# Performance work log

Hardware: AMD Instinct MI355X
Metric: run time of the kernel (lower is better)

Reference implementation:

```python
import jax, jax.numpy as jnp
import numpy as np

N_NODES = 50000
N_EDGES = 200000
IN_FEATS = 32
OUT_FEATS = 32
EDGE_DIM = 16


def setup_inputs() -> dict:
    key = jax.random.key(0)
    k1, k2, k3, k4, k5 = jax.random.split(key, 5)
    feat = jax.random.normal(k1, (N_NODES, IN_FEATS), dtype=jnp.float32)
    efeat = jax.random.normal(k2, (N_EDGES, EDGE_DIM), dtype=jnp.float32)
    src = jax.random.randint(k3, (N_EDGES,), 0, N_NODES, dtype=jnp.int32)
    dst = jax.random.randint(k4, (N_EDGES,), 0, N_NODES, dtype=jnp.int32)
    # edge_func = Linear(EDGE_DIM -> IN_FEATS*OUT_FEATS)
    W_edge = jax.random.normal(k5, (EDGE_DIM, IN_FEATS * OUT_FEATS), dtype=jnp.float32) * (1.0 / np.sqrt(EDGE_DIM))
    b_edge = jnp.zeros((IN_FEATS * OUT_FEATS,), dtype=jnp.float32)
    bias = jnp.zeros((OUT_FEATS,), dtype=jnp.float32)
    return {"feat": feat, "efeat": efeat, "src": src, "dst": dst,
            "W_edge": W_edge, "b_edge": b_edge, "bias": bias}


def reference(feat, efeat, src, dst, W_edge, b_edge, bias):
    # edge_func: (E, edge_dim) -> (E, in, out) edge-conditioned weights
    w = (efeat @ W_edge + b_edge).reshape(-1, IN_FEATS, OUT_FEATS)
    # u_mul_e + sum over in dim  ==  per-edge matvec: h_src[e] @ W[e]
    h_src = feat[src]                               # (E, in) gather
    msg = jnp.einsum('ei,eio->eo', h_src, w)        # (E, out)
    # mean reduce over incoming edges per destination node
    agg = jax.ops.segment_sum(msg, dst, num_segments=N_NODES)   # (N, out)
    deg = jax.ops.segment_sum(jnp.ones((msg.shape[0],), dtype=msg.dtype), dst,
                              num_segments=N_NODES)
    agg = agg / jnp.maximum(deg, 1.0)[:, None]      # zero-degree nodes stay 0
    return agg + bias
```

## Files before the change

kernel.cpp:

```cpp
#include <hip/hip_runtime.h>
#include <hip/hip_bf16.h>

#define NNODES 50000
#define NEDGES 200000
#define WCT_ROW 552
#define WCT_BYTES (32 * WCT_ROW * 2)
#define HROW 40
#define TILE_EDGES 64
#define NTILES (NEDGES / TILE_EDGES)
#define GEMM_BLOCKS ((NTILES + 1) / 2)
#define CHAIN_BLKS ((NEDGES + 255) / 256)
#define DROW 33

#define MSG_OFF   0
#define HEAD_OFF  25600000
#define NEXT_OFF  25800000
#define WCT_OFF   26600000

using f32x4 = __attribute__((ext_vector_type(4))) float;
using f16x2 = __attribute__((ext_vector_type(2))) _Float16;
using f16x4 = __attribute__((ext_vector_type(4))) _Float16;
using f16x8 = __attribute__((ext_vector_type(8))) _Float16;

__device__ __forceinline__ f16x2 pkrtz(float a, float b) {
    return __builtin_bit_cast(f16x2, __builtin_amdgcn_cvt_pkrtz(a, b));
}

__device__ __forceinline__ void gload_lds16(const void* g, void* l) {
    __builtin_amdgcn_global_load_lds(
        (const __attribute__((address_space(1))) unsigned int*)g,
        (__attribute__((address_space(3))) unsigned int*)l, 16, 0, 0);
}

#define WCT_BLKS 69
__global__ void init_kernel(const float* __restrict__ W_edge,
                            const float* __restrict__ b_edge,
                            _Float16* __restrict__ wct,
                            unsigned* __restrict__ head) {
    int b = blockIdx.x;
    if (b < WCT_BLKS) {
        int gid = b * 256 + threadIdx.x;
        if (gid >= 32 * WCT_ROW) return;
        int n = gid / WCT_ROW;
        int c = gid - n * WCT_ROW;
        float v = 0.0f;
        if (c < 512)      v = W_edge[(c & 15) * 1024 + (c >> 4) * 32 + n];
        else if (c < 544) v = b_edge[(c - 512) * 32 + n];
        wct[gid] = (_Float16)v;
    } else {
        int gid = (b - WCT_BLKS) * 256 + threadIdx.x;
        if (gid < NNODES) head[gid] = 0xFFFFFFFFu;
    }
}

__global__ __launch_bounds__(256, 3) void work_kernel(
    const float* __restrict__ feat, const float* __restrict__ efeat,
    const int* __restrict__ src, const int* __restrict__ dst,
    const _Float16* __restrict__ wct_g,
    float4* __restrict__ msg4, unsigned* __restrict__ head,
    unsigned* __restrict__ next) {

    __shared__ __align__(16) unsigned short wct_lds[32 * WCT_ROW];
    __shared__ __align__(16) unsigned short h_lds[TILE_EDGES * HROW];
    __shared__ __align__(16) float dtile[TILE_EDGES * DROW];

    const int t = threadIdx.x;

    if (blockIdx.x >= GEMM_BLOCKS) {
        int e = (blockIdx.x - GEMM_BLOCKS) * 256 + t;
        if (e < NEDGES)
            next[e] = atomicExch(&head[dst[e]], (unsigned)e);
        return;
    }

    const int lane = t & 63;
    const int wave = t >> 6;
    const int tile0 = blockIdx.x * 2;
    const int tile1 = tile0 + 1;
    const bool has1 = (tile1 < NTILES);
    const int ebase0 = tile0 * TILE_EDGES;
    const int ebase1 = tile1 * TILE_EDGES;

    const int r16 = lane & 15;
    const int g   = lane >> 4;
    const int wbase = wave * 16;
    const int et = t >> 2, p = t & 3;

    {
        const char* gsrc = (const char*)wct_g;
        char* lbase = (char*)wct_lds;
        #pragma unroll
        for (int c = 0; c < 9; ++c) {
            int chunk = wave + c * 4;
            if (chunk < 35) {
                int boff = (chunk << 10) + lane * 16;
                if (boff < WCT_BYTES) gload_lds16(gsrc + boff, lbase + boff);
            }
        }
    }

    const int se0 = src[ebase0 + et];
    int se1 = 0;
    if (has1) se1 = src[ebase1 + et];

    float4 ef0a, ef0b, ef1a, ef1b;
    {
        const float* efp = efeat + (ebase0 + wbase + r16) * 16 + (g & 1) * 8;
        ef0a = *(const float4*)efp;
        ef0b = *(const float4*)(efp + 4);
    }
    if (has1) {
        const float* efp = efeat + (ebase1 + wbase + r16) * 16 + (g & 1) * 8;
        ef1a = *(const float4*)efp;
        ef1b = *(const float4*)(efp + 4);
    }

    {
        const float* fp = feat + se0 * 32 + p * 8;
        float4 a = *(const float4*)fp;
        float4 b = *(const float4*)(fp + 4);
        uint4 hp;
        hp.x = __builtin_bit_cast(unsigned int, pkrtz(a.x, a.y));
        hp.y = __builtin_bit_cast(unsigned int, pkrtz(a.z, a.w));
        hp.z = __builtin_bit_cast(unsigned int, pkrtz(b.x, b.y));
        hp.w = __builtin_bit_cast(unsigned int, pkrtz(b.z, b.w));
        *(uint4*)(void*)(h_lds + et * HROW + p * 8) = hp;
    }

    f16x2 ef2[4] = { pkrtz(ef0a.x, ef0a.y), pkrtz(ef0a.z, ef0a.w),
                     pkrtz(ef0b.x, ef0b.y), pkrtz(ef0b.z, ef0b.w) };

    __syncthreads();

    const _Float16* brow0 = (const _Float16*)wct_lds + r16 * WCT_ROW;
    const _Float16* brow1 = (const _Float16*)wct_lds + (16 + r16) * WCT_ROW;

    unsigned int hbc[16];
    f16x8 af_bias;
    {
        const uint4* hrow = (const uint4*)(void*)(h_lds + (wbase + r16) * HROW);
        unsigned int hw[16];
        #pragma unroll
        for (int q = 0; q < 4; ++q) {
            uint4 v = hrow[q];
            hw[q*4+0] = v.x; hw[q*4+1] = v.y; hw[q*4+2] = v.z; hw[q*4+3] = v.w;
        }
        const bool hi = (g >> 1) & 1;
        #pragma unroll
        for (int s = 0; s < 16; ++s) {
            unsigned int x = hi ? (hw[s] >> 16) : (hw[s] & 0xffffu);
            hbc[s] = x | (x << 16);
        }
        af_bias = *(const f16x8*)(void*)((const _Float16*)h_lds + (wbase + r16) * HROW + g * 8);
    }

    float4 f1a = {0,0,0,0}, f1b = {0,0,0,0};
    if (has1) {
        const float* fp = feat + se1 * 32 + p * 8;
        f1a = *(const float4*)fp;
        f1b = *(const float4*)(fp + 4);
    }

    f32x4 acc0 = {0.f, 0.f, 0.f, 0.f};
    f32x4 acc1 = {0.f, 0.f, 0.f, 0.f};

    #pragma unroll
    for (int s = 0; s < 16; ++s) {
        const int koff = s * 32 + g * 8;
        f16x8 b0 = *(const f16x8*)(brow0 + koff);
        f16x8 b1 = *(const f16x8*)(brow1 + koff);
        f16x2 hb = __builtin_bit_cast(f16x2, hbc[s]);
        f16x2 p0 = hb * ef2[0], p1 = hb * ef2[1], p2 = hb * ef2[2], p3 = hb * ef2[3];
        f16x4 lo  = __builtin_shufflevector(p0, p1, 0, 1, 2, 3);
        f16x4 hi4 = __builtin_shufflevector(p2, p3, 0, 1, 2, 3);
        f16x8 af  = __builtin_shufflevector(lo, hi4, 0, 1, 2, 3, 4, 5, 6, 7);
        acc0 = __builtin_amdgcn_mfma_f32_16x16x32_f16(af, b0, acc0, 0, 0, 0);
        acc1 = __builtin_amdgcn_mfma_f32_16x16x32_f16(af, b1, acc1, 0, 0, 0);
    }
    {
        const int koff = 512 + g * 8;
        f16x8 b0 = *(const f16x8*)(brow0 + koff);
        f16x8 b1 = *(const f16x8*)(brow1 + koff);
        acc0 = __builtin_amdgcn_mfma_f32_16x16x32_f16(af_bias, b0, acc0, 0, 0, 0);
        acc1 = __builtin_amdgcn_mfma_f32_16x16x32_f16(af_bias, b1, acc1, 0, 0, 0);
    }

    {
        const int browD = wbase + g * 4;
        #pragma unroll
        for (int r = 0; r < 4; ++r) {
            dtile[(browD + r) * DROW + r16]      = acc0[r];
            dtile[(browD + r) * DROW + 16 + r16] = acc1[r];
        }
    }
    asm volatile("s_waitcnt lgkmcnt(0)" ::: "memory");
    __builtin_amdgcn_sched_barrier(0);
    {
        const int rA = wbase + (lane >> 3);
        const int cA = (lane & 7) * 4;
        float4 vA = *(const float4*)(dtile + rA * DROW + cA);
        float4 vB = *(const float4*)(dtile + (rA + 8) * DROW + cA);
        float4* mp = msg4 + (size_t)ebase0 * 8 + wave * 128;
        mp[lane]      = vA;
        mp[64 + lane] = vB;
    }

    if (!has1) return;

    {
        uint4 hp;
        hp.x = __builtin_bit_cast(unsigned int, pkrtz(f1a.x, f1a.y));
        hp.y = __builtin_bit_cast(unsigned int, pkrtz(f1a.z, f1a.w));
        hp.z = __builtin_bit_cast(unsigned int, pkrtz(f1b.x, f1b.y));
        hp.w = __builtin_bit_cast(unsigned int, pkrtz(f1b.z, f1b.w));
        *(uint4*)(void*)(h_lds + et * HROW + p * 8) = hp;
    }
    asm volatile("s_waitcnt lgkmcnt(0)" ::: "memory");
    __builtin_amdgcn_sched_barrier(0);

    ef2[0] = pkrtz(ef1a.x, ef1a.y); ef2[1] = pkrtz(ef1a.z, ef1a.w);
    ef2[2] = pkrtz(ef1b.x, ef1b.y); ef2[3] = pkrtz(ef1b.z, ef1b.w);

    {
        const uint4* hrow = (const uint4*)(void*)(h_lds + (wbase + r16) * HROW);
        unsigned int hw[16];
        #pragma unroll
        for (int q = 0; q < 4; ++q) {
            uint4 v = hrow[q];
            hw[q*4+0] = v.x; hw[q*4+1] = v.y; hw[q*4+2] = v.z; hw[q*4+3] = v.w;
        }
        const bool hi = (g >> 1) & 1;
        #pragma unroll
        for (int s = 0; s < 16; ++s) {
            unsigned int x = hi ? (hw[s] >> 16) : (hw[s] & 0xffffu);
            hbc[s] = x | (x << 16);
        }
        af_bias = *(const f16x8*)(void*)((const _Float16*)h_lds + (wbase + r16) * HROW + g * 8);
    }

    acc0 = (f32x4){0.f, 0.f, 0.f, 0.f};
    acc1 = (f32x4){0.f, 0.f, 0.f, 0.f};

    #pragma unroll
    for (int s = 0; s < 16; ++s) {
        const int koff = s * 32 + g * 8;
        f16x8 b0 = *(const f16x8*)(brow0 + koff);
        f16x8 b1 = *(const f16x8*)(brow1 + koff);
        f16x2 hb = __builtin_bit_cast(f16x2, hbc[s]);
        f16x2 p0 = hb * ef2[0], p1 = hb * ef2[1], p2 = hb * ef2[2], p3 = hb * ef2[3];
        f16x4 lo  = __builtin_shufflevector(p0, p1, 0, 1, 2, 3);
        f16x4 hi4 = __builtin_shufflevector(p2, p3, 0, 1, 2, 3);
        f16x8 af  = __builtin_shufflevector(lo, hi4, 0, 1, 2, 3, 4, 5, 6, 7);
        acc0 = __builtin_amdgcn_mfma_f32_16x16x32_f16(af, b0, acc0, 0, 0, 0);
        acc1 = __builtin_amdgcn_mfma_f32_16x16x32_f16(af, b1, acc1, 0, 0, 0);
    }
    {
        const int koff = 512 + g * 8;
        f16x8 b0 = *(const f16x8*)(brow0 + koff);
        f16x8 b1 = *(const f16x8*)(brow1 + koff);
        acc0 = __builtin_amdgcn_mfma_f32_16x16x32_f16(af_bias, b0, acc0, 0, 0, 0);
        acc1 = __builtin_amdgcn_mfma_f32_16x16x32_f16(af_bias, b1, acc1, 0, 0, 0);
    }

    {
        const int browD = wbase + g * 4;
        #pragma unroll
        for (int r = 0; r < 4; ++r) {
            dtile[(browD + r) * DROW + r16]      = acc0[r];
            dtile[(browD + r) * DROW + 16 + r16] = acc1[r];
        }
    }
    asm volatile("s_waitcnt lgkmcnt(0)" ::: "memory");
    __builtin_amdgcn_sched_barrier(0);
    {
        const int rA = wbase + (lane >> 3);
        const int cA = (lane & 7) * 4;
        float4 vA = *(const float4*)(dtile + rA * DROW + cA);
        float4 vB = *(const float4*)(dtile + (rA + 8) * DROW + cA);
        float4* mp = msg4 + (size_t)ebase1 * 8 + wave * 128;
        mp[lane]      = vA;
        mp[64 + lane] = vB;
    }
}

__global__ __launch_bounds__(256) void pull_kernel(
    const float4* __restrict__ msg4, const unsigned* __restrict__ head,
    const unsigned* __restrict__ next, const float* __restrict__ bias,
    float* __restrict__ out) {

    int gid = blockIdx.x * 256 + threadIdx.x;
    if (gid >= NNODES * 8) return;
    int n = gid >> 3, Q = gid & 7;

    float4 s = {0.f, 0.f, 0.f, 0.f};
    float degf = 0.0f;

    unsigned e = head[n];
    while (e != 0xFFFFFFFFu) {
        float4 m = msg4[(size_t)e * 8 + Q];
        s.x += m.x; s.y += m.y; s.z += m.z; s.w += m.w;
        degf += 1.0f;
        e = next[e];
    }

    float inv = 1.0f / fmaxf(degf, 1.0f);
    float4 b = ((const float4*)bias)[Q];
    float4 o = { s.x * inv + b.x, s.y * inv + b.y, s.z * inv + b.z, s.w * inv + b.w };
    *(float4*)(out + n * 32 + Q * 4) = o;
}

extern "C" void kernel_launch(void* const* d_in, const int* in_sizes, int n_in,
                              void* d_out, int out_size, void* d_ws, size_t ws_size,
                              hipStream_t stream) {
    const float* feat   = (const float*)d_in[0];
    const float* efeat  = (const float*)d_in[1];
    const int*   src    = (const int*)d_in[2];
    const int*   dst    = (const int*)d_in[3];
    const float* W_edge = (const float*)d_in[4];
    const float* b_edge = (const float*)d_in[5];
    const float* bias   = (const float*)d_in[6];

    char* ws = (char*)d_ws;
    float4*   msg4 = (float4*)(ws + MSG_OFF);
    unsigned* head = (unsigned*)(ws + HEAD_OFF);
    unsigned* next = (unsigned*)(ws + NEXT_OFF);
    _Float16* wct  = (_Float16*)(ws + WCT_OFF);
    float*    out  = (float*)d_out;

    init_kernel<<<WCT_BLKS + (NNODES + 255) / 256, 256, 0, stream>>>(
        W_edge, b_edge, wct, head);
    work_kernel<<<GEMM_BLOCKS + CHAIN_BLKS, 256, 0, stream>>>(
        feat, efeat, src, dst, wct, msg4, head, next);
    pull_kernel<<<(NNODES * 8 + 255) / 256, 256, 0, stream>>>(
        msg4, head, next, bias, out);
}
```

Before: 40.82 us.

## Fold linked-list build into GEMM blocks and store MFMA output directly

Removes the separate chain-building blocks and has the first 128 threads of each GEMM block do the atomicExch list insertion for that block's two tiles. It also drops the LDS transpose tile and writes MFMA accumulators straight to global memory with strided scalar stores. The smaller LDS footprint allows raising launch bounds to 4 blocks per CU. The trade-off is less coalesced message stores and atomic latency now interleaved inside the GEMM blocks.

```diff
diff --git a/kernel.cpp b/kernel.cpp
--- a/kernel.cpp
+++ b/kernel.cpp
@@ -9,8 +9,6 @@
 #define TILE_EDGES 64
 #define NTILES (NEDGES / TILE_EDGES)
 #define GEMM_BLOCKS ((NTILES + 1) / 2)
-#define CHAIN_BLKS ((NEDGES + 255) / 256)
-#define DROW 33
 
 #define MSG_OFF   0
 #define HEAD_OFF  25600000
@@ -53,26 +51,17 @@
     }
 }
 
-__global__ __launch_bounds__(256, 3) void work_kernel(
+__global__ __launch_bounds__(256, 4) void work_kernel(
     const float* __restrict__ feat, const float* __restrict__ efeat,
     const int* __restrict__ src, const int* __restrict__ dst,
     const _Float16* __restrict__ wct_g,
-    float4* __restrict__ msg4, unsigned* __restrict__ head,
+    float* __restrict__ msg, unsigned* __restrict__ head,
     unsigned* __restrict__ next) {
 
     __shared__ __align__(16) unsigned short wct_lds[32 * WCT_ROW];
     __shared__ __align__(16) unsigned short h_lds[TILE_EDGES * HROW];
-    __shared__ __align__(16) float dtile[TILE_EDGES * DROW];
 
     const int t = threadIdx.x;
-
-    if (blockIdx.x >= GEMM_BLOCKS) {
-        int e = (blockIdx.x - GEMM_BLOCKS) * 256 + t;
-        if (e < NEDGES)
-            next[e] = atomicExch(&head[dst[e]], (unsigned)e);
-        return;
-    }
-
     const int lane = t & 63;
     const int wave = t >> 6;
     const int tile0 = blockIdx.x * 2;
@@ -99,11 +88,17 @@
         }
     }
 
+    if (t < 2 * TILE_EDGES) {
+        int e = ebase0 + t;
+        if (e < NEDGES)
+            next[e] = atomicExch(&head[dst[e]], (unsigned)e);
+    }
+
     const int se0 = src[ebase0 + et];
     int se1 = 0;
     if (has1) se1 = src[ebase1 + et];
 
-    float4 ef0a, ef0b, ef1a, ef1b;
+    float4 ef0a, ef0b, ef1a = {0,0,0,0}, ef1b = {0,0,0,0};
     {
         const float* efp = efeat + (ebase0 + wbase + r16) * 16 + (g & 1) * 8;
         ef0a = *(const float4*)efp;
@@ -186,23 +181,12 @@
     }
 
     {
-        const int browD = wbase + g * 4;
+        float* mrow = msg + (size_t)(ebase0 + wbase + g * 4) * 32 + r16;
         #pragma unroll
         for (int r = 0; r < 4; ++r) {
-            dtile[(browD + r) * DROW + r16]      = acc0[r];
-            dtile[(browD + r) * DROW + 16 + r16] = acc1[r];
-        }
-    }
-    asm volatile("s_waitcnt lgkmcnt(0)" ::: "memory");
-    __builtin_amdgcn_sched_barrier(0);
-    {
-        const int rA = wbase + (lane >> 3);
-        const int cA = (lane & 7) * 4;
-        float4 vA = *(const float4*)(dtile + rA * DROW + cA);
-        float4 vB = *(const float4*)(dtile + (rA + 8) * DROW + cA);
-        float4* mp = msg4 + (size_t)ebase0 * 8 + wave * 128;
-        mp[lane]      = vA;
-        mp[64 + lane] = vB;
+            mrow[r * 32]      = acc0[r];
+            mrow[r * 32 + 16] = acc1[r];
+        }
     }
 
     if (!has1) return;
@@ -263,23 +247,12 @@
     }
 
     {
-        const int browD = wbase + g * 4;
+        float* mrow = msg + (size_t)(ebase1 + wbase + g * 4) * 32 + r16;
         #pragma unroll
         for (int r = 0; r < 4; ++r) {
-            dtile[(browD + r) * DROW + r16]      = acc0[r];
-            dtile[(browD + r) * DROW + 16 + r16] = acc1[r];
-        }
-    }
-    asm volatile("s_waitcnt lgkmcnt(0)" ::: "memory");
-    __builtin_amdgcn_sched_barrier(0);
-    {
-        const int rA = wbase + (lane >> 3);
-        const int cA = (lane & 7) * 4;
-        float4 vA = *(const float4*)(dtile + rA * DROW + cA);
-        float4 vB = *(const float4*)(dtile + (rA + 8) * DROW + cA);
-        float4* mp = msg4 + (size_t)ebase1 * 8 + wave * 128;
-        mp[lane]      = vA;
-        mp[64 + lane] = vB;
+            mrow[r * 32]      = acc0[r];
+            mrow[r * 32 + 16] = acc1[r];
+        }
     }
 }
 
@@ -321,7 +294,7 @@
     const float* bias   = (const float*)d_in[6];
 
     char* ws = (char*)d_ws;
-    float4*   msg4 = (float4*)(ws + MSG_OFF);
+    float*    msg  = (float*)(ws + MSG_OFF);
     unsigned* head = (unsigned*)(ws + HEAD_OFF);
     unsigned* next = (unsigned*)(ws + NEXT_OFF);
     _Float16* wct  = (_Float16*)(ws + WCT_OFF);
@@ -329,8 +302,8 @@
 
     init_kernel<<<WCT_BLKS + (NNODES + 255) / 256, 256, 0, stream>>>(
         W_edge, b_edge, wct, head);
-    work_kernel<<<GEMM_BLOCKS + CHAIN_BLKS, 256, 0, stream>>>(
-        feat, efeat, src, dst, wct, msg4, head, next);
+    work_kernel<<<GEMM_BLOCKS, 256, 0, stream>>>(
+        feat, efeat, src, dst, wct, msg, head, next);
     pull_kernel<<<(NNODES * 8 + 255) / 256, 256, 0, stream>>>(
-        msg4, head, next, bias, out);
-}
+        (const float4*)msg, head, next, bias, out);
+}
```

Measured after the change: 41.00 us. About the same (+0.4%).
